# Kernel tuning notes

Hardware: AMD Instinct MI355X
Metric: run time of the kernel (lower is better)

## Reference

```python
import jax, jax.numpy as jnp
import numpy as np

B, T, A, G, E, H = 64, 128, 30, 3, 64, 256
FA, FE, NE = 32, 16, 30
LA = A * 36
SD = A * FA + NE * FE + LA  # 2520


def setup_inputs() -> dict:
    key = jax.random.key(0)
    ks = iter(jax.random.split(key, 64))
    p = lambda *s: jax.random.normal(next(ks), s, jnp.float32) * 0.02
    qvals = jax.random.normal(next(ks), (B, T, A), jnp.float32)
    # ally states with a valid one-hot group type in the last G slots (constant over t)
    ally = jax.random.normal(next(ks), (B, T, A, FA), jnp.float32)
    grp = jax.random.randint(next(ks), (B, A), 0, G)
    onehot = jax.nn.one_hot(grp, G, dtype=jnp.float32)  # (B,A,G)
    ally = ally.at[:, :, :, -G:].set(jnp.broadcast_to(onehot[:, None], (B, T, A, G)))
    rest = jax.random.normal(next(ks), (B, T, NE * FE + LA), jnp.float32)
    states = jnp.concatenate([ally.reshape(B, T, A * FA), rest], axis=2)
    d = {"qvals": qvals, "states": states}
    d["g_w1_W1"] = p(G, SD, H); d["g_w1_b1"] = p(G, H); d["g_w1_W2"] = p(G, H, A * E); d["g_w1_b2"] = p(G, A * E)
    d["g_b1_W1"] = p(G, SD, H); d["g_b1_b1"] = p(G, H); d["g_b1_W2"] = p(G, H, E); d["g_b1_b2"] = p(G, E)
    d["g_w2_W1"] = p(G, SD, H); d["g_w2_b1"] = p(G, H); d["g_w2_W2"] = p(G, H, E); d["g_w2_b2"] = p(G, E)
    d["g_b2_W1"] = p(G, SD, E); d["g_b2_b1"] = p(G, E); d["g_b2_W2"] = p(G, E, 1); d["g_b2_b2"] = p(G, 1)
    d["h_w1_W1"] = p(SD, H); d["h_w1_b1"] = p(H); d["h_w1_W2"] = p(H, G * E); d["h_w1_b2"] = p(G * E)
    d["h_b1_W1"] = p(SD, H); d["h_b1_b1"] = p(H); d["h_b1_W2"] = p(H, E); d["h_b1_b2"] = p(E)
    d["h_w2_W1"] = p(SD, H); d["h_w2_b1"] = p(H); d["h_w2_W2"] = p(H, E); d["h_w2_b2"] = p(E)
    d["h_b2_W1"] = p(SD, E); d["h_b2_b1"] = p(E); d["h_b2_W2"] = p(E, 1); d["h_b2_b2"] = p(1)
    return d


def reference(qvals, states,
              g_w1_W1, g_w1_b1, g_w1_W2, g_w1_b2,
              g_b1_W1, g_b1_b1, g_b1_W2, g_b1_b2,
              g_w2_W1, g_w2_b1, g_w2_W2, g_w2_b2,
              g_b2_W1, g_b2_b1, g_b2_W2, g_b2_b2,
              h_w1_W1, h_w1_b1, h_w1_W2, h_w1_b2,
              h_b1_W1, h_b1_b1, h_b1_W2, h_b1_b2,
              h_w2_W1, h_w2_b1, h_w2_W2, h_w2_b2,
              h_b2_W1, h_b2_b1, h_b2_W2, h_b2_b2):
    N = B * T
    s = states.reshape(N, SD)
    # group masks from the one-hot type slots at t=0 (constant across time)
    ally = states[..., : A * FA].reshape(B, T, A, FA)
    type0 = ally[:, 0, :, -G:]                                  # (B,A,G)
    masks = jnp.transpose(type0 == 1.0, (2, 0, 1)).astype(qvals.dtype)  # (G,B,A)
    mq = (qvals[None] * masks[:, :, None, :]).reshape(G, N, A)  # (G,N,A)

    def gmlp(W1, b1, W2, b2):  # stacked-over-groups 2-layer MLP
        h = jax.nn.relu(jnp.einsum('nd,gdh->gnh', s, W1) + b1[:, None])
        return jnp.einsum('gnh,gho->gno', h, W2) + b2[:, None]

    w1 = jnp.abs(gmlp(g_w1_W1, g_w1_b1, g_w1_W2, g_w1_b2)).reshape(G, N, A, E)
    b1 = gmlp(g_b1_W1, g_b1_b1, g_b1_W2, g_b1_b2)               # (G,N,E)
    w2 = jnp.abs(gmlp(g_w2_W1, g_w2_b1, g_w2_W2, g_w2_b2))      # (G,N,E)
    b2 = gmlp(g_b2_W1, g_b2_b1, g_b2_W2, g_b2_b2)[..., 0]       # (G,N)
    hidden = jax.nn.elu(jnp.einsum('gna,gnae->gne', mq, w1) + b1)
    group_qvals = (jnp.einsum('gne,gne->gn', hidden, w2) + b2).T  # (N,G)

    def hmlp(W1, b1_, W2, b2_):
        return jax.nn.relu(s @ W1 + b1_) @ W2 + b2_

    hw1 = jnp.abs(hmlp(h_w1_W1, h_w1_b1, h_w1_W2, h_w1_b2)).reshape(N, G, E)
    hb1 = hmlp(h_b1_W1, h_b1_b1, h_b1_W2, h_b1_b2)              # (N,E)
    hw2 = jnp.abs(hmlp(h_w2_W1, h_w2_b1, h_w2_W2, h_w2_b2))     # (N,E)
    hb2 = hmlp(h_b2_W1, h_b2_b1, h_b2_W2, h_b2_b2)[:, 0]        # (N,)
    hid = jax.nn.elu(jnp.einsum('ng,nge->ne', group_qvals, hw1) + hb1)
    qtot = jnp.einsum('ne,ne->n', hid, hw2) + hb2
    return qtot.reshape(B, T, 1)
```

## Files before the change

### kernel.cpp

```cpp
#include <hip/hip_runtime.h>

typedef unsigned short u16;
typedef __bf16 bf16x8 __attribute__((ext_vector_type(8)));
typedef float f32x4 __attribute__((ext_vector_type(4)));
typedef unsigned short u16x8 __attribute__((ext_vector_type(8)));

#define NB 64
#define NT 128
#define NA 30
#define NG 3
#define NE 64
#define NH 256
#define NN 8192
#define SD 2520
#define KP 2560
#define NC 3328
#define NKT 40
#define NITER 20

__device__ __forceinline__ u16 f2bf(float f) {
  union { float f; unsigned u; } c; c.f = f;
  unsigned u = c.u + 0x7FFFu + ((c.u >> 16) & 1u);
  return (u16)(u >> 16);
}
__device__ __forceinline__ float bf2f(u16 h) {
  union { unsigned u; float f; } c; c.u = ((unsigned)h) << 16;
  return c.f;
}
__device__ __forceinline__ float eluf(float x) { return x > 0.f ? x : expm1f(x); }

__device__ __forceinline__ void gload16(const u16* g, u16* l) {
  __builtin_amdgcn_global_load_lds((const __attribute__((address_space(1))) void*)g,
                                   (__attribute__((address_space(3))) void*)l, 16, 0, 0);
}

__device__ __forceinline__ float wredsum(float v) {
  #pragma unroll
  for (int d = 32; d > 0; d >>= 1) v += __shfl_xor(v, d, 64);
  return v;
}

__global__ __launch_bounds__(256) void pack_all_k(
    const float* __restrict__ states,
    const float* __restrict__ gw1W1, const float* __restrict__ gw1b1,
    const float* __restrict__ gb1W1, const float* __restrict__ gb1b1,
    const float* __restrict__ gw2W1, const float* __restrict__ gw2b1,
    const float* __restrict__ gb2W1, const float* __restrict__ gb2b1,
    const float* __restrict__ hw1W1, const float* __restrict__ hw1b1,
    const float* __restrict__ hb1W1, const float* __restrict__ hb1b1,
    const float* __restrict__ hw2W1, const float* __restrict__ hw2b1,
    const float* __restrict__ hb2W1, const float* __restrict__ hb2b1,
    const float* __restrict__ gw1W2, const float* __restrict__ gb1W2,
    const float* __restrict__ gw2W2, const float* __restrict__ hw1W2,
    const float* __restrict__ hb1W2, const float* __restrict__ hw2W2,
    u16* __restrict__ A, u16* __restrict__ BT, float* __restrict__ bias,
    u16* __restrict__ w2tw1, u16* __restrict__ w2ts,
    int* __restrict__ grps, int* __restrict__ gcnt) {
  int bid = blockIdx.x;
  if (bid < 10240) {
    int tid = bid * 256 + threadIdx.x;
    int n = tid / 320, kq = tid - n * 320;
    int k = kq * 8;
    u16x8 v;
    if (k < SD) {
      const float4* p = reinterpret_cast<const float4*>(states + (size_t)n * SD + k);
      float4 x0 = p[0], x1 = p[1];
      v[0]=f2bf(x0.x); v[1]=f2bf(x0.y); v[2]=f2bf(x0.z); v[3]=f2bf(x0.w);
      v[4]=f2bf(x1.x); v[5]=f2bf(x1.y); v[6]=f2bf(x1.z); v[7]=f2bf(x1.w);
    } else {
      v[0]=0;v[1]=0;v[2]=0;v[3]=0;v[4]=0;v[5]=0;v[6]=0;v[7]=0;
    }
    *reinterpret_cast<u16x8*>(A + (size_t)n * KP + k) = v;
  } else if (bid < 14400) {
    int tid = (bid - 10240) * 256 + threadIdx.x;
    int kq = tid / NC, j = tid - kq * NC;
    const float* W; const float* bsrc; size_t cbase; int stride; int q;
    if (j < 768)        { q=j;      int g=q>>8; W=gw1W1; cbase=(size_t)g*SD*NH + (q&255); stride=NH; bsrc=gw1b1; }
    else if (j < 1536)  { q=j-768;  int g=q>>8; W=gb1W1; cbase=(size_t)g*SD*NH + (q&255); stride=NH; bsrc=gb1b1; }
    else if (j < 2304)  { q=j-1536; int g=q>>8; W=gw2W1; cbase=(size_t)g*SD*NH + (q&255); stride=NH; bsrc=gw2b1; }
    else if (j < 2496)  { q=j-2304; int g=q>>6; W=gb2W1; cbase=(size_t)g*SD*NE + (q&63);  stride=NE; bsrc=gb2b1; }
    else if (j < 2752)  { q=j-2496; W=hw1W1; cbase=q; stride=NH; bsrc=hw1b1; }
    else if (j < 3008)  { q=j-2752; W=hb1W1; cbase=q; stride=NH; bsrc=hb1b1; }
    else if (j < 3264)  { q=j-3008; W=hw2W1; cbase=q; stride=NH; bsrc=hw2b1; }
    else                { q=j-3264; W=hb2W1; cbase=q; stride=NE; bsrc=hb2b1; }
    int k = kq * 8;
    u16x8 v;
    #pragma unroll
    for (int i = 0; i < 8; ++i) {
      int d = k + i;
      v[i] = (d < SD) ? f2bf(W[cbase + (size_t)d * stride]) : (u16)0;
    }
    *reinterpret_cast<u16x8*>(BT + (size_t)j * KP + k) = v;
    if (kq == 0) bias[j] = bsrc[q];
  } else if (bid < 15120) {
    int tid = (bid - 14400) * 256 + threadIdx.x;
    int lane = tid & 63, cf = (tid >> 6) & 3, ks = (tid >> 8) & 7, slab = tid >> 11;
    int g = slab / 30, a = slab - g * 30;
    int e = cf * 16 + (lane & 15);
    int h0 = ks * 32 + (lane >> 4) * 8;
    const float* src = gw1W2 + (size_t)g * (NH * 1920) + (size_t)h0 * 1920 + a * 64 + e;
    u16x8 v;
    #pragma unroll
    for (int i = 0; i < 8; ++i) v[i] = f2bf(src[(size_t)i * 1920]);
    *reinterpret_cast<u16x8*>(w2tw1 + (size_t)tid * 8) = v;
  } else if (bid < 15208) {
    int tid = (bid - 15120) * 256 + threadIdx.x;
    int lane = tid & 63, cf = (tid >> 6) & 3, ks = (tid >> 8) & 7, u = tid >> 11;
    int e = cf * 16 + (lane & 15);
    int h0 = ks * 32 + (lane >> 4) * 8;
    const float* src; int stride;
    if (u < 3)       { src = gb1W2 + (size_t)u * (NH*NE) + (size_t)h0 * NE + e;     stride = NE; }
    else if (u < 6)  { src = gw2W2 + (size_t)(u-3) * (NH*NE) + (size_t)h0 * NE + e; stride = NE; }
    else if (u < 9)  { src = hw1W2 + (size_t)h0 * (NG*NE) + (u-6)*64 + e;           stride = NG*NE; }
    else if (u == 9) { src = hb1W2 + (size_t)h0 * NE + e;                           stride = NE; }
    else             { src = hw2W2 + (size_t)h0 * NE + e;                           stride = NE; }
    u16x8 v;
    #pragma unroll
    for (int i = 0; i < 8; ++i) v[i] = f2bf(src[(size_t)i * stride]);
    *reinterpret_cast<u16x8*>(w2ts + (size_t)tid * 8) = v;
  } else {
    int b = threadIdx.x;
    if (b >= NB) return;
    int gv0 = 0, gv1 = 0;
    int cnt0 = 0, cnt1 = 0, cnt2 = 0;
    #pragma unroll
    for (int a = 0; a < NA; ++a) {
      int g = 0;
      #pragma unroll
      for (int gi = 0; gi < NG; ++gi)
        if (states[(size_t)b * NT * SD + a * 32 + 29 + gi] == 1.0f) g = gi;
      if (a < 15) gv0 |= g << (2 * a); else gv1 |= g << (2 * (a - 15));
      if (g == 0) ++cnt0; else if (g == 1) ++cnt1; else ++cnt2;
    }
    gcnt[b * 4 + 0] = cnt0; gcnt[b * 4 + 1] = cnt1; gcnt[b * 4 + 2] = cnt2;
    int off0 = 0, off1 = cnt0, off2 = cnt0 + cnt1;
    #pragma unroll
    for (int a = 0; a < NA; ++a) {
      int g = (a < 15) ? ((gv0 >> (2 * a)) & 3) : ((gv1 >> (2 * (a - 15))) & 3);
      int pos;
      if (g == 0) pos = off0++; else if (g == 1) pos = off1++; else pos = off2++;
      grps[b * NA + pos] = a;
    }
  }
}

__global__ __launch_bounds__(512, 2) void gemm1_k(const u16* __restrict__ A, const u16* __restrict__ BT,
    const float* __restrict__ bias, u16* __restrict__ act) {
  __shared__ u16 lds[65536];
  int t = threadIdx.x;
  int wg = blockIdx.x;
  int swz = (wg & 7) * 52 + (wg >> 3);
  int by = swz / 13, bx = swz - by * 13;
  size_t mb = (size_t)by * 256, nb = (size_t)bx * 256;
  int lane = t & 63, w = t >> 6;
  int wm = (w >> 2) * 128;
  int wn = (w & 3) * 64;
  int l15 = lane & 15, hi = lane >> 4;

  int srow = t >> 3;
  int scol = (((t & 7) ^ (srow & 7)) << 3);
  const u16* aS = A + (mb + srow) * KP + scol;
  const u16* bS = BT + (nb + srow) * KP + scol;

#define STGA(buf, h, kt) { \
    u16* d_ = lds + (buf) * 32768 + (h) * 8192; \
    const u16* s_ = aS + (size_t)((h) * 128) * KP + (size_t)(kt) * 64; \
    gload16(s_,                  d_ + t * 8); \
    gload16(s_ + (size_t)64 * KP, d_ + 4096 + t * 8); }
#define STGB(buf, h, kt) { \
    u16* d_ = lds + (buf) * 32768 + 16384 + (h) * 8192; \
    const u16* s_ = bS + (size_t)((h) * 128) * KP + (size_t)(kt) * 64; \
    gload16(s_,                  d_ + t * 8); \
    gload16(s_ + (size_t)64 * KP, d_ + 4096 + t * 8); }

  f32x4 acc[8][4];
  #pragma unroll
  for (int mi = 0; mi < 8; ++mi)
    #pragma unroll
    for (int ni = 0; ni < 4; ++ni) acc[mi][ni] = {0.f, 0.f, 0.f, 0.f};

  const char* A0 = (const char*)(lds) + (wm ? 16384 : 0);
  const char* B0 = (const char*)(lds) + 32768 + ((wn & 128) ? 16384 : 0);
  const char* A1 = A0 + 65536;
  const char* B1 = B0 + 65536;
  int rx = l15 & 7;
  int aBase = l15 * 128;
  int bBase = ((wn & 64) + l15) * 128;
  int slot0 = (hi ^ rx) << 4;
  int slot1 = ((4 + hi) ^ rx) << 4;

  bf16x8 afA[4][2], afB[4][2], bfA[2][2], bfB[2][2];

#define LD_AFA(Ab) { _Pragma("unroll") for (int m_ = 0; m_ < 4; ++m_) { \
    afA[m_][0] = *reinterpret_cast<const bf16x8*>((Ab) + aBase + m_ * 2048 + slot0); \
    afA[m_][1] = *reinterpret_cast<const bf16x8*>((Ab) + aBase + m_ * 2048 + slot1); } }
#define LD_AFB(Ab) { _Pragma("unroll") for (int m_ = 0; m_ < 4; ++m_) { \
    afB[m_][0] = *reinterpret_cast<const bf16x8*>((Ab) + aBase + (4 + m_) * 2048 + slot0); \
    afB[m_][1] = *reinterpret_cast<const bf16x8*>((Ab) + aBase + (4 + m_) * 2048 + slot1); } }
#define LD_BFA(Bb) { _Pragma("unroll") for (int n_ = 0; n_ < 2; ++n_) { \
    bfA[n_][0] = *reinterpret_cast<const bf16x8*>((Bb) + bBase + n_ * 2048 + slot0); \
    bfA[n_][1] = *reinterpret_cast<const bf16x8*>((Bb) + bBase + n_ * 2048 + slot1); } }
#define LD_BFB(Bb) { _Pragma("unroll") for (int n_ = 0; n_ < 2; ++n_) { \
    bfB[n_][0] = *reinterpret_cast<const bf16x8*>((Bb) + bBase + (2 + n_) * 2048 + slot0); \
    bfB[n_][1] = *reinterpret_cast<const bf16x8*>((Bb) + bBase + (2 + n_) * 2048 + slot1); } }
#define MM_Q(AF, BF, MO, NO) { _Pragma("unroll") for (int m_ = 0; m_ < 4; ++m_) \
    _Pragma("unroll") for (int n_ = 0; n_ < 2; ++n_) { \
      acc[(MO)+m_][(NO)+n_] = __builtin_amdgcn_mfma_f32_16x16x32_bf16(AF[m_][0], BF[n_][0], acc[(MO)+m_][(NO)+n_], 0, 0, 0); \
      acc[(MO)+m_][(NO)+n_] = __builtin_amdgcn_mfma_f32_16x16x32_bf16(AF[m_][1], BF[n_][1], acc[(MO)+m_][(NO)+n_], 0, 0, 0); } }
#define SYNC_IN  __builtin_amdgcn_s_barrier(); \
                 asm volatile("s_waitcnt lgkmcnt(0)" ::: "memory"); \
                 __builtin_amdgcn_sched_barrier(0); \
                 __builtin_amdgcn_s_setprio(1);
#define SYNC_OUT __builtin_amdgcn_s_setprio(0); \
                 __builtin_amdgcn_s_barrier(); \
                 asm volatile("" ::: "memory");

  STGA(0, 0, 0); STGA(0, 1, 0); STGB(0, 0, 0); STGB(0, 1, 0);
  STGB(1, 0, 1); STGB(1, 1, 1);
  asm volatile("s_waitcnt vmcnt(4)" ::: "memory");
  __builtin_amdgcn_s_barrier();
  asm volatile("" ::: "memory");

  for (int it = 0; it < NITER; ++it) {
    int k1 = 2 * it + 1;
    bool t2 = (2 * it + 2 < NKT), t3 = (2 * it + 3 < NKT);
    LD_AFA(A0); LD_BFA(B0);
    STGA(1, 0, k1);
    SYNC_IN; MM_Q(afA, bfA, 0, 0); SYNC_OUT;
    LD_BFB(B0);
    STGA(1, 1, k1);
    SYNC_IN; MM_Q(afA, bfB, 0, 2); SYNC_OUT;
    LD_AFB(A0);
    if (t2) STGB(0, 0, 2 * it + 2);
    SYNC_IN; MM_Q(afB, bfB, 4, 2); SYNC_OUT;
    if (t2) STGB(0, 1, 2 * it + 2);
    __builtin_amdgcn_s_barrier();
    __builtin_amdgcn_s_setprio(1); MM_Q(afB, bfA, 4, 0); __builtin_amdgcn_s_setprio(0);
    if (it == NITER - 1) { asm volatile("s_waitcnt vmcnt(0)" ::: "memory"); }
    else                 { asm volatile("s_waitcnt vmcnt(4)" ::: "memory"); }
    __builtin_amdgcn_s_barrier();
    asm volatile("" ::: "memory");
    LD_AFA(A1); LD_BFA(B1);
    if (t2) STGA(0, 0, 2 * it + 2);
    SYNC_IN; MM_Q(afA, bfA, 0, 0); SYNC_OUT;
    LD_BFB(B1);
    if (t2) STGA(0, 1, 2 * it + 2);
    SYNC_IN; MM_Q(afA, bfB, 0, 2); SYNC_OUT;
    LD_AFB(A1);
    if (t3) STGB(1, 0, 2 * it + 3);
    SYNC_IN; MM_Q(afB, bfB, 4, 2); SYNC_OUT;
    if (t3) STGB(1, 1, 2 * it + 3);
    __builtin_amdgcn_s_barrier();
    __builtin_amdgcn_s_setprio(1); MM_Q(afB, bfA, 4, 0); __builtin_amdgcn_s_setprio(0);
    if (t3) { asm volatile("s_waitcnt vmcnt(4)" ::: "memory"); }
    __builtin_amdgcn_s_barrier();
    asm volatile("" ::: "memory");
  }

  int r00 = (int)mb + wm + hi * 4;
  int cc0 = (int)nb + wn + l15;
  float bv0 = bias[cc0], bv1 = bias[cc0 + 16], bv2 = bias[cc0 + 32], bv3 = bias[cc0 + 48];
  #pragma unroll
  for (int mi = 0; mi < 8; ++mi) {
    #pragma unroll
    for (int i = 0; i < 4; ++i) {
      u16* dst = act + (size_t)(r00 + mi * 16 + i) * NC + cc0;
      float v0 = acc[mi][0][i] + bv0; v0 = v0 > 0.f ? v0 : 0.f;
      float v1 = acc[mi][1][i] + bv1; v1 = v1 > 0.f ? v1 : 0.f;
      float v2 = acc[mi][2][i] + bv2; v2 = v2 > 0.f ? v2 : 0.f;
      float v3 = acc[mi][3][i] + bv3; v3 = v3 > 0.f ? v3 : 0.f;
      dst[0] = f2bf(v0); dst[16] = f2bf(v1); dst[32] = f2bf(v2); dst[48] = f2bf(v3);
    }
  }
#undef STGA
#undef STGB
#undef LD_AFA
#undef LD_AFB
#undef LD_BFA
#undef LD_BFB
#undef MM_Q
#undef SYNC_IN
#undef SYNC_OUT
}

__global__ __launch_bounds__(128) void c1a_k(const u16* __restrict__ act, const float* __restrict__ qvals,
    const int* __restrict__ grps, const int* __restrict__ gcnt, const u16* __restrict__ w2tw1,
    const float* __restrict__ gw1b2, float* __restrict__ qw1acc) {
  int t = threadIdx.x, lane = t & 63, w = t >> 6;
  int rb = blockIdx.x;
  int g = blockIdx.y;
  int nb0 = rb * 32 + w * 16;
  int b = rb >> 2;
  int l16 = lane & 15, lk8 = (lane >> 4) * 8;
  int cnt0 = gcnt[b * 4], cnt1 = gcnt[b * 4 + 1], cnt2 = gcnt[b * 4 + 2];
  int start = (g >= 1 ? cnt0 : 0) + (g >= 2 ? cnt1 : 0);
  int cnt = (g == 0) ? cnt0 : (g == 1) ? cnt1 : cnt2;
  float gacc[4][4];
  #pragma unroll
  for (int cf = 0; cf < 4; ++cf)
    #pragma unroll
    for (int i = 0; i < 4; ++i) gacc[cf][i] = 0.f;
  const u16* arow = act + (size_t)(nb0 + l16) * NC;
  int r4 = nb0 + (lane >> 4) * 4;
  const u16* abase = arow + g * NH;
  bf16x8 af0[4], af1[4];
  #pragma unroll
  for (int ks = 0; ks < 4; ++ks) {
    af0[ks] = *reinterpret_cast<const bf16x8*>(abase + ks * 32 + lk8);
    af1[ks] = *reinterpret_cast<const bf16x8*>(abase + (4 + ks) * 32 + lk8);
  }
  const int* sl = grps + b * NA + start;
  for (int ai = 0; ai < cnt; ++ai) {
    int a = sl[ai];
    f32x4 t4[4], u4[4];
    #pragma unroll
    for (int cf = 0; cf < 4; ++cf) { t4[cf] = {0.f,0.f,0.f,0.f}; u4[cf] = {0.f,0.f,0.f,0.f}; }
    const u16* bbase = w2tw1 + (size_t)(g * NA + a) * 16384 + lane * 8;
    #pragma unroll
    for (int ks = 0; ks < 4; ++ks) {
      #pragma unroll
      for (int cf = 0; cf < 4; ++cf) {
        bf16x8 bf0 = *reinterpret_cast<const bf16x8*>(bbase + (ks * 4 + cf) * 512);
        bf16x8 bf1 = *reinterpret_cast<const bf16x8*>(bbase + ((4 + ks) * 4 + cf) * 512);
        t4[cf] = __builtin_amdgcn_mfma_f32_16x16x32_bf16(af0[ks], bf0, t4[cf], 0, 0, 0);
        u4[cf] = __builtin_amdgcn_mfma_f32_16x16x32_bf16(af1[ks], bf1, u4[cf], 0, 0, 0);
      }
    }
    float qv[4];
    #pragma unroll
    for (int i = 0; i < 4; ++i) qv[i] = qvals[(size_t)(r4 + i) * NA + a];
    const float* bias = gw1b2 + (size_t)g * (NA * NE) + a * NE;
    #pragma unroll
    for (int cf = 0; cf < 4; ++cf) {
      float bv = bias[cf*16 + l16];
      #pragma unroll
      for (int i = 0; i < 4; ++i) gacc[cf][i] += qv[i] * fabsf(t4[cf][i] + u4[cf][i] + bv);
    }
  }
  #pragma unroll
  for (int cf = 0; cf < 4; ++cf)
    #pragma unroll
    for (int i = 0; i < 4; ++i)
      qw1acc[(size_t)(r4 + i) * 192 + g * 64 + cf * 16 + l16] = gacc[cf][i];
}

__global__ __launch_bounds__(256) void c1b_k(const u16* __restrict__ act, const u16* __restrict__ w2ts,
    const float* __restrict__ gb1b2, const float* __restrict__ gw2b2, const float* __restrict__ hw1b2,
    const float* __restrict__ hb1b2, const float* __restrict__ hw2b2,
    float* __restrict__ b1s, float* __restrict__ w2s, float* __restrict__ hw1s,
    float* __restrict__ hb1s, float* __restrict__ hw2s) {
  int u = blockIdx.x, blk = blockIdx.y;
  int t = threadIdx.x, lane = t & 63, w = t >> 6;
  int nb0 = blk * 64 + w * 16;
  int l16 = lane & 15, lk8 = (lane >> 4) * 8;
  int aoff = (u < 3) ? 768 + u * 256 : (u < 6) ? 1536 + (u-3) * 256 : (u < 9) ? 2496 : (u == 9) ? 2752 : 3008;
  const float* bias; float* outp; int ostride; bool ab;
  if (u < 3)       { bias = gb1b2 + u * 64;       outp = b1s  + u * 64;     ostride = 192; ab = false; }
  else if (u < 6)  { bias = gw2b2 + (u-3) * 64;   outp = w2s  + (u-3) * 64; ostride = 192; ab = true; }
  else if (u < 9)  { bias = hw1b2 + (u-6) * 64;   outp = hw1s + (u-6) * 64; ostride = 192; ab = true; }
  else if (u == 9) { bias = hb1b2;                outp = hb1s;              ostride = 64;  ab = false; }
  else             { bias = hw2b2;                outp = hw2s;              ostride = 64;  ab = true; }
  f32x4 t4[4];
  #pragma unroll
  for (int cf = 0; cf < 4; ++cf) t4[cf] = {0.f, 0.f, 0.f, 0.f};
  const u16* arow = act + (size_t)(nb0 + l16) * NC + aoff;
  const u16* bbase = w2ts + (size_t)u * 16384 + lane * 8;
  #pragma unroll
  for (int ks = 0; ks < 8; ++ks) {
    bf16x8 af = *reinterpret_cast<const bf16x8*>(arow + ks * 32 + lk8);
    #pragma unroll
    for (int cf = 0; cf < 4; ++cf) {
      bf16x8 bf = *reinterpret_cast<const bf16x8*>(bbase + (ks * 4 + cf) * 512);
      t4[cf] = __builtin_amdgcn_mfma_f32_16x16x32_bf16(af, bf, t4[cf], 0, 0, 0);
    }
  }
  int r4 = nb0 + (lane >> 4) * 4;
  #pragma unroll
  for (int cf = 0; cf < 4; ++cf) {
    float bv = bias[cf*16 + l16];
    #pragma unroll
    for (int i = 0; i < 4; ++i) {
      float v = t4[cf][i] + bv;
      if (ab) v = fabsf(v);
      outp[(size_t)(r4 + i) * ostride + cf * 16 + l16] = v;
    }
  }
}

__global__ __launch_bounds__(256) void c2_k(const u16* __restrict__ act,
    const float* __restrict__ qw1acc, const float* __restrict__ b1s, const float* __restrict__ w2s,
    const float* __restrict__ hw1s, const float* __restrict__ hb1s, const float* __restrict__ hw2s,
    const float* __restrict__ gb2W2, const float* __restrict__ gb2b2,
    const float* __restrict__ hb2W2, const float* __restrict__ hb2b2,
    float* __restrict__ out) {
  int gtid = blockIdx.x * 256 + threadIdx.x;
  int n = gtid >> 6, e = gtid & 63;
  const u16* an = act + (size_t)n * NC;
  const float* qn = qw1acc + (size_t)n * 192;
  float q0 = qn[e], q1 = qn[64 + e], q2 = qn[128 + e];
  const float* b1n = b1s + (size_t)n * 192;
  const float* w2n = w2s + (size_t)n * 192;
  float s0 = bf2f(an[2304 + e]) * gb2W2[e]       + eluf(q0 + b1n[e])       * w2n[e];
  float s1 = bf2f(an[2368 + e]) * gb2W2[64 + e]  + eluf(q1 + b1n[64 + e])  * w2n[64 + e];
  float s2 = bf2f(an[2432 + e]) * gb2W2[128 + e] + eluf(q2 + b1n[128 + e]) * w2n[128 + e];
  float sh = bf2f(an[3264 + e]) * hb2W2[e];
  float gq0 = wredsum(s0) + gb2b2[0];
  float gq1 = wredsum(s1) + gb2b2[1];
  float gq2 = wredsum(s2) + gb2b2[2];
  float hb2v = wredsum(sh) + hb2b2[0];
  const float* hw1n = hw1s + (size_t)n * 192;
  float hv = gq0 * hw1n[e] + gq1 * hw1n[64 + e] + gq2 * hw1n[128 + e] + hb1s[(size_t)n * 64 + e];
  float c = eluf(hv) * hw2s[(size_t)n * 64 + e];
  float qt = wredsum(c) + hb2v;
  if (e == 0) out[n] = qt;
}

extern "C" void kernel_launch(void* const* d_in, const int* in_sizes, int n_in,
                              void* d_out, int out_size, void* d_ws, size_t ws_size,
                              hipStream_t stream) {
  const float* qvals  = (const float*)d_in[0];
  const float* states = (const float*)d_in[1];
  const float* gw1W1 = (const float*)d_in[2];
  const float* gw1b1 = (const float*)d_in[3];
  const float* gw1W2 = (const float*)d_in[4];
  const float* gw1b2 = (const float*)d_in[5];
  const float* gb1W1 = (const float*)d_in[6];
  const float* gb1b1 = (const float*)d_in[7];
  const float* gb1W2 = (const float*)d_in[8];
  const float* gb1b2 = (const float*)d_in[9];
  const float* gw2W1 = (const float*)d_in[10];
  const float* gw2b1 = (const float*)d_in[11];
  const float* gw2W2 = (const float*)d_in[12];
  const float* gw2b2 = (const float*)d_in[13];
  const float* gb2W1 = (const float*)d_in[14];
  const float* gb2b1 = (const float*)d_in[15];
  const float* gb2W2 = (const float*)d_in[16];
  const float* gb2b2 = (const float*)d_in[17];
  const float* hw1W1 = (const float*)d_in[18];
  const float* hw1b1 = (const float*)d_in[19];
  const float* hw1W2 = (const float*)d_in[20];
  const float* hw1b2 = (const float*)d_in[21];
  const float* hb1W1 = (const float*)d_in[22];
  const float* hb1b1 = (const float*)d_in[23];
  const float* hb1W2 = (const float*)d_in[24];
  const float* hb1b2 = (const float*)d_in[25];
  const float* hw2W1 = (const float*)d_in[26];
  const float* hw2b1 = (const float*)d_in[27];
  const float* hw2W2 = (const float*)d_in[28];
  const float* hw2b2 = (const float*)d_in[29];
  const float* hb2W1 = (const float*)d_in[30];
  const float* hb2b1 = (const float*)d_in[31];
  const float* hb2W2 = (const float*)d_in[32];
  const float* hb2b2 = (const float*)d_in[33];
  float* out = (float*)d_out;

  char* p = (char*)d_ws;
  u16* A       = (u16*)p;   p += (size_t)NN * KP * 2;
  u16* BT      = (u16*)p;   p += (size_t)NC * KP * 2;
  u16* act     = (u16*)p;   p += (size_t)NN * NC * 2;
  u16* w2tw1   = (u16*)p;   p += (size_t)5760 * NH * 2;
  u16* w2ts    = (u16*)p;   p += (size_t)704 * NH * 2;
  float* bias  = (float*)p; p += (size_t)NC * 4;
  int* grps    = (int*)p;   p += (size_t)NB * NA * 4;
  int* gcnt    = (int*)p;   p += (size_t)NB * 4 * 4;
  float* b1s   = (float*)p; p += (size_t)NN * 192 * 4;
  float* w2s   = (float*)p; p += (size_t)NN * 192 * 4;
  float* hw1s  = (float*)p; p += (size_t)NN * 192 * 4;
  float* hb1s  = (float*)p; p += (size_t)NN * 64 * 4;
  float* hw2s  = (float*)p; p += (size_t)NN * 64 * 4;
  float* qw1acc = (float*)A;

  pack_all_k<<<15209, 256, 0, stream>>>(states,
                                        gw1W1, gw1b1, gb1W1, gb1b1, gw2W1, gw2b1, gb2W1, gb2b1,
                                        hw1W1, hw1b1, hb1W1, hb1b1, hw2W1, hw2b1, hb2W1, hb2b1,
                                        gw1W2, gb1W2, gw2W2, hw1W2, hb1W2, hw2W2,
                                        A, BT, bias, w2tw1, w2ts, grps, gcnt);
  gemm1_k<<<416, 512, 0, stream>>>(A, BT, bias, act);
  c1a_k<<<dim3(256, 3), 128, 0, stream>>>(act, qvals, grps, gcnt, w2tw1, gw1b2, qw1acc);
  c1b_k<<<dim3(11, 128), 256, 0, stream>>>(act, w2ts, gb1b2, gw2b2, hw1b2, hb1b2, hw2b2,
                                           b1s, w2s, hw1s, hb1s, hw2s);
  c2_k<<<2048, 256, 0, stream>>>(act, qw1acc, b1s, w2s, hw1s, hb1s, hw2s,
                                 gb2W2, gb2b2, hb2W2, hb2b2, out);
}
```

Before: 237.2 us.

## Fuse second-layer hypernet GEMMs with final mixing into one kernel

Merges c1b_k and c2_k into a single kernel that computes the eleven small second-layer MFMA products per 16-row tile and consumes them directly in registers for the group and hyper mixing. The b2 dot products become an extra MFMA unit packed into w2ts, replacing the wave reductions. This removes the fp32 intermediate buffers (b1s, w2s, hw1s, hb1s, hw2s) and their global write and reread traffic, plus one launch. In exchange the fused kernel runs only 128 blocks with serial per-wave work, so parallelism and occupancy are much lower.

```diff
diff --git a/kernel.cpp b/kernel.cpp
--- a/kernel.cpp
+++ b/kernel.cpp
@@ -32,12 +32,6 @@
 __device__ __forceinline__ void gload16(const u16* g, u16* l) {
   __builtin_amdgcn_global_load_lds((const __attribute__((address_space(1))) void*)g,
                                    (__attribute__((address_space(3))) void*)l, 16, 0, 0);
-}
-
-__device__ __forceinline__ float wredsum(float v) {
-  #pragma unroll
-  for (int d = 32; d > 0; d >>= 1) v += __shfl_xor(v, d, 64);
-  return v;
 }
 
 __global__ __launch_bounds__(256) void pack_all_k(
@@ -53,6 +47,7 @@
     const float* __restrict__ gw1W2, const float* __restrict__ gb1W2,
     const float* __restrict__ gw2W2, const float* __restrict__ hw1W2,
     const float* __restrict__ hb1W2, const float* __restrict__ hw2W2,
+    const float* __restrict__ gb2W2, const float* __restrict__ hb2W2,
     u16* __restrict__ A, u16* __restrict__ BT, float* __restrict__ bias,
     u16* __restrict__ w2tw1, u16* __restrict__ w2ts,
     int* __restrict__ grps, int* __restrict__ gcnt) {
@@ -103,20 +98,31 @@
     #pragma unroll
     for (int i = 0; i < 8; ++i) v[i] = f2bf(src[(size_t)i * 1920]);
     *reinterpret_cast<u16x8*>(w2tw1 + (size_t)tid * 8) = v;
-  } else if (bid < 15208) {
+  } else if (bid < 15216) {
     int tid = (bid - 15120) * 256 + threadIdx.x;
     int lane = tid & 63, cf = (tid >> 6) & 3, ks = (tid >> 8) & 7, u = tid >> 11;
-    int e = cf * 16 + (lane & 15);
+    int c = cf * 16 + (lane & 15);
     int h0 = ks * 32 + (lane >> 4) * 8;
-    const float* src; int stride;
-    if (u < 3)       { src = gb1W2 + (size_t)u * (NH*NE) + (size_t)h0 * NE + e;     stride = NE; }
-    else if (u < 6)  { src = gw2W2 + (size_t)(u-3) * (NH*NE) + (size_t)h0 * NE + e; stride = NE; }
-    else if (u < 9)  { src = hw1W2 + (size_t)h0 * (NG*NE) + (u-6)*64 + e;           stride = NG*NE; }
-    else if (u == 9) { src = hb1W2 + (size_t)h0 * NE + e;                           stride = NE; }
-    else             { src = hw2W2 + (size_t)h0 * NE + e;                           stride = NE; }
     u16x8 v;
-    #pragma unroll
-    for (int i = 0; i < 8; ++i) v[i] = f2bf(src[(size_t)i * stride]);
+    if (u < 11) {
+      const float* src; int stride;
+      if (u < 3)       { src = gb1W2 + (size_t)u * (NH*NE) + (size_t)h0 * NE + c;     stride = NE; }
+      else if (u < 6)  { src = gw2W2 + (size_t)(u-3) * (NH*NE) + (size_t)h0 * NE + c; stride = NE; }
+      else if (u < 9)  { src = hw1W2 + (size_t)h0 * (NG*NE) + (u-6)*64 + c;           stride = NG*NE; }
+      else if (u == 9) { src = hb1W2 + (size_t)h0 * NE + c;                           stride = NE; }
+      else             { src = hw2W2 + (size_t)h0 * NE + c;                           stride = NE; }
+      #pragma unroll
+      for (int i = 0; i < 8; ++i) v[i] = f2bf(src[(size_t)i * stride]);
+    } else {
+      #pragma unroll
+      for (int i = 0; i < 8; ++i) {
+        int k = h0 + i;
+        float val = 0.f;
+        if (ks < 6) { if (c == k / 64) val = gb2W2[k]; }
+        else        { int kk = k - 192; if (c == 3) val = hb2W2[kk]; }
+        v[i] = f2bf(val);
+      }
+    }
     *reinterpret_cast<u16x8*>(w2ts + (size_t)tid * 8) = v;
   } else {
     int b = threadIdx.x;
@@ -344,75 +350,121 @@
       qw1acc[(size_t)(r4 + i) * 192 + g * 64 + cf * 16 + l16] = gacc[cf][i];
 }
 
-__global__ __launch_bounds__(256) void c1b_k(const u16* __restrict__ act, const u16* __restrict__ w2ts,
+__global__ __launch_bounds__(256) void c1bc2_k(const u16* __restrict__ act,
+    const float* __restrict__ qw1acc, const u16* __restrict__ w2ts,
     const float* __restrict__ gb1b2, const float* __restrict__ gw2b2, const float* __restrict__ hw1b2,
     const float* __restrict__ hb1b2, const float* __restrict__ hw2b2,
-    float* __restrict__ b1s, float* __restrict__ w2s, float* __restrict__ hw1s,
-    float* __restrict__ hb1s, float* __restrict__ hw2s) {
-  int u = blockIdx.x, blk = blockIdx.y;
+    const float* __restrict__ gb2b2, const float* __restrict__ hb2b2,
+    float* __restrict__ out) {
   int t = threadIdx.x, lane = t & 63, w = t >> 6;
-  int nb0 = blk * 64 + w * 16;
-  int l16 = lane & 15, lk8 = (lane >> 4) * 8;
-  int aoff = (u < 3) ? 768 + u * 256 : (u < 6) ? 1536 + (u-3) * 256 : (u < 9) ? 2496 : (u == 9) ? 2752 : 3008;
-  const float* bias; float* outp; int ostride; bool ab;
-  if (u < 3)       { bias = gb1b2 + u * 64;       outp = b1s  + u * 64;     ostride = 192; ab = false; }
-  else if (u < 6)  { bias = gw2b2 + (u-3) * 64;   outp = w2s  + (u-3) * 64; ostride = 192; ab = true; }
-  else if (u < 9)  { bias = hw1b2 + (u-6) * 64;   outp = hw1s + (u-6) * 64; ostride = 192; ab = true; }
-  else if (u == 9) { bias = hb1b2;                outp = hb1s;              ostride = 64;  ab = false; }
-  else             { bias = hw2b2;                outp = hw2s;              ostride = 64;  ab = true; }
-  f32x4 t4[4];
-  #pragma unroll
-  for (int cf = 0; cf < 4; ++cf) t4[cf] = {0.f, 0.f, 0.f, 0.f};
-  const u16* arow = act + (size_t)(nb0 + l16) * NC + aoff;
-  const u16* bbase = w2ts + (size_t)u * 16384 + lane * 8;
-  #pragma unroll
-  for (int ks = 0; ks < 8; ++ks) {
-    bf16x8 af = *reinterpret_cast<const bf16x8*>(arow + ks * 32 + lk8);
+  int nb0 = blockIdx.x * 64 + w * 16;
+  int l16 = lane & 15, hi = lane >> 4, lk8 = hi * 8;
+  const u16* arow = act + (size_t)(nb0 + l16) * NC;
+  int r4 = nb0 + hi * 4;
+
+#define UNIT(u_, aoff_, res_) { \
+    f32x4 t4_[4]; \
+    _Pragma("unroll") for (int cf = 0; cf < 4; ++cf) t4_[cf] = {0.f,0.f,0.f,0.f}; \
+    const u16* bb_ = w2ts + (size_t)(u_) * 16384 + lane * 8; \
+    _Pragma("unroll") for (int ks = 0; ks < 8; ++ks) { \
+      bf16x8 af_ = *reinterpret_cast<const bf16x8*>(arow + (aoff_) + ks * 32 + lk8); \
+      _Pragma("unroll") for (int cf = 0; cf < 4; ++cf) { \
+        bf16x8 bf_ = *reinterpret_cast<const bf16x8*>(bb_ + (ks * 4 + cf) * 512); \
+        t4_[cf] = __builtin_amdgcn_mfma_f32_16x16x32_bf16(af_, bf_, t4_[cf], 0, 0, 0); \
+      } } \
+    _Pragma("unroll") for (int cf = 0; cf < 4; ++cf) res_[cf] = t4_[cf]; }
+
+#define GRED(x) { x += __shfl_xor(x, 1, 64); x += __shfl_xor(x, 2, 64); \
+                  x += __shfl_xor(x, 4, 64); x += __shfl_xor(x, 8, 64); }
+
+  f32x4 d4 = {0.f, 0.f, 0.f, 0.f};
+  {
+    const u16* bb = w2ts + (size_t)11 * 16384 + lane * 8;
+    #pragma unroll
+    for (int ks = 0; ks < 8; ++ks) {
+      int aoff = (ks < 6) ? (2304 + ks * 32) : (3264 + (ks - 6) * 32);
+      bf16x8 af = *reinterpret_cast<const bf16x8*>(arow + aoff + lk8);
+      bf16x8 bf = *reinterpret_cast<const bf16x8*>(bb + (ks * 4) * 512);
+      d4 = __builtin_amdgcn_mfma_f32_16x16x32_bf16(af, bf, d4, 0, 0, 0);
+    }
+  }
+  float dotn[4][4];
+  #pragma unroll
+  for (int n = 0; n < 4; ++n)
+    #pragma unroll
+    for (int i = 0; i < 4; ++i)
+      dotn[n][i] = __shfl(d4[i], (lane & 48) + n, 64);
+
+  float gq[3][4];
+  #pragma unroll
+  for (int g = 0; g < 3; ++g) {
+    f32x4 b1r[4], w2r[4];
+    UNIT(g, 768 + g * 256, b1r);
+    UNIT(3 + g, 1536 + g * 256, w2r);
+    float part[4] = {0.f, 0.f, 0.f, 0.f};
     #pragma unroll
     for (int cf = 0; cf < 4; ++cf) {
-      bf16x8 bf = *reinterpret_cast<const bf16x8*>(bbase + (ks * 4 + cf) * 512);
-      t4[cf] = __builtin_amdgcn_mfma_f32_16x16x32_bf16(af, bf, t4[cf], 0, 0, 0);
-    }
-  }
-  int r4 = nb0 + (lane >> 4) * 4;
+      float b1b = gb1b2[g * 64 + cf * 16 + l16];
+      float w2b = gw2b2[g * 64 + cf * 16 + l16];
+      #pragma unroll
+      for (int i = 0; i < 4; ++i) {
+        float q = qw1acc[(size_t)(r4 + i) * 192 + g * 64 + cf * 16 + l16];
+        part[i] += eluf(q + b1r[cf][i] + b1b) * fabsf(w2r[cf][i] + w2b);
+      }
+    }
+    #pragma unroll
+    for (int i = 0; i < 4; ++i) {
+      GRED(part[i]);
+      gq[g][i] = part[i] + dotn[g][i] + gb2b2[g];
+    }
+  }
+
+  f32x4 h6[4], h7[4], h8[4], h9[4], h10[4];
+  {
+    f32x4 t6[4], t7[4], t8[4];
+    #pragma unroll
+    for (int cf = 0; cf < 4; ++cf) { t6[cf] = {0.f,0.f,0.f,0.f}; t7[cf] = {0.f,0.f,0.f,0.f}; t8[cf] = {0.f,0.f,0.f,0.f}; }
+    const u16* bb6 = w2ts + (size_t)6 * 16384 + lane * 8;
+    const u16* bb7 = w2ts + (size_t)7 * 16384 + lane * 8;
+    const u16* bb8 = w2ts + (size_t)8 * 16384 + lane * 8;
+    #pragma unroll
+    for (int ks = 0; ks < 8; ++ks) {
+      bf16x8 af = *reinterpret_cast<const bf16x8*>(arow + 2496 + ks * 32 + lk8);
+      #pragma unroll
+      for (int cf = 0; cf < 4; ++cf) {
+        t6[cf] = __builtin_amdgcn_mfma_f32_16x16x32_bf16(af, *reinterpret_cast<const bf16x8*>(bb6 + (ks*4+cf)*512), t6[cf], 0, 0, 0);
+        t7[cf] = __builtin_amdgcn_mfma_f32_16x16x32_bf16(af, *reinterpret_cast<const bf16x8*>(bb7 + (ks*4+cf)*512), t7[cf], 0, 0, 0);
+        t8[cf] = __builtin_amdgcn_mfma_f32_16x16x32_bf16(af, *reinterpret_cast<const bf16x8*>(bb8 + (ks*4+cf)*512), t8[cf], 0, 0, 0);
+      }
+    }
+    #pragma unroll
+    for (int cf = 0; cf < 4; ++cf) { h6[cf] = t6[cf]; h7[cf] = t7[cf]; h8[cf] = t8[cf]; }
+  }
+  UNIT(9, 2752, h9);
+  UNIT(10, 3008, h10);
+
+  float qtp[4] = {0.f, 0.f, 0.f, 0.f};
   #pragma unroll
   for (int cf = 0; cf < 4; ++cf) {
-    float bv = bias[cf*16 + l16];
+    int e = cf * 16 + l16;
+    float b6 = hw1b2[e], b7 = hw1b2[64 + e], b8 = hw1b2[128 + e];
+    float b9 = hb1b2[e], b10 = hw2b2[e];
     #pragma unroll
     for (int i = 0; i < 4; ++i) {
-      float v = t4[cf][i] + bv;
-      if (ab) v = fabsf(v);
-      outp[(size_t)(r4 + i) * ostride + cf * 16 + l16] = v;
-    }
-  }
-}
-
-__global__ __launch_bounds__(256) void c2_k(const u16* __restrict__ act,
-    const float* __restrict__ qw1acc, const float* __restrict__ b1s, const float* __restrict__ w2s,
-    const float* __restrict__ hw1s, const float* __restrict__ hb1s, const float* __restrict__ hw2s,
-    const float* __restrict__ gb2W2, const float* __restrict__ gb2b2,
-    const float* __restrict__ hb2W2, const float* __restrict__ hb2b2,
-    float* __restrict__ out) {
-  int gtid = blockIdx.x * 256 + threadIdx.x;
-  int n = gtid >> 6, e = gtid & 63;
-  const u16* an = act + (size_t)n * NC;
-  const float* qn = qw1acc + (size_t)n * 192;
-  float q0 = qn[e], q1 = qn[64 + e], q2 = qn[128 + e];
-  const float* b1n = b1s + (size_t)n * 192;
-  const float* w2n = w2s + (size_t)n * 192;
-  float s0 = bf2f(an[2304 + e]) * gb2W2[e]       + eluf(q0 + b1n[e])       * w2n[e];
-  float s1 = bf2f(an[2368 + e]) * gb2W2[64 + e]  + eluf(q1 + b1n[64 + e])  * w2n[64 + e];
-  float s2 = bf2f(an[2432 + e]) * gb2W2[128 + e] + eluf(q2 + b1n[128 + e]) * w2n[128 + e];
-  float sh = bf2f(an[3264 + e]) * hb2W2[e];
-  float gq0 = wredsum(s0) + gb2b2[0];
-  float gq1 = wredsum(s1) + gb2b2[1];
-  float gq2 = wredsum(s2) + gb2b2[2];
-  float hb2v = wredsum(sh) + hb2b2[0];
-  const float* hw1n = hw1s + (size_t)n * 192;
-  float hv = gq0 * hw1n[e] + gq1 * hw1n[64 + e] + gq2 * hw1n[128 + e] + hb1s[(size_t)n * 64 + e];
-  float c = eluf(hv) * hw2s[(size_t)n * 64 + e];
-  float qt = wredsum(c) + hb2v;
-  if (e == 0) out[n] = qt;
+      float hv = gq[0][i] * fabsf(h6[cf][i] + b6)
+               + gq[1][i] * fabsf(h7[cf][i] + b7)
+               + gq[2][i] * fabsf(h8[cf][i] + b8)
+               + h9[cf][i] + b9;
+      qtp[i] += eluf(hv) * fabsf(h10[cf][i] + b10);
+    }
+  }
+  #pragma unroll
+  for (int i = 0; i < 4; ++i) {
+    GRED(qtp[i]);
+    if (l16 == 0) out[r4 + i] = qtp[i] + dotn[3][i] + hb2b2[0];
+  }
+#undef UNIT
+#undef GRED
 }
 
 extern "C" void kernel_launch(void* const* d_in, const int* in_sizes, int n_in,
@@ -459,26 +511,19 @@
   u16* BT      = (u16*)p;   p += (size_t)NC * KP * 2;
   u16* act     = (u16*)p;   p += (size_t)NN * NC * 2;
   u16* w2tw1   = (u16*)p;   p += (size_t)5760 * NH * 2;
-  u16* w2ts    = (u16*)p;   p += (size_t)704 * NH * 2;
+  u16* w2ts    = (u16*)p;   p += (size_t)12 * 16384 * 2;
   float* bias  = (float*)p; p += (size_t)NC * 4;
   int* grps    = (int*)p;   p += (size_t)NB * NA * 4;
   int* gcnt    = (int*)p;   p += (size_t)NB * 4 * 4;
-  float* b1s   = (float*)p; p += (size_t)NN * 192 * 4;
-  float* w2s   = (float*)p; p += (size_t)NN * 192 * 4;
-  float* hw1s  = (float*)p; p += (size_t)NN * 192 * 4;
-  float* hb1s  = (float*)p; p += (size_t)NN * 64 * 4;
-  float* hw2s  = (float*)p; p += (size_t)NN * 64 * 4;
   float* qw1acc = (float*)A;
 
-  pack_all_k<<<15209, 256, 0, stream>>>(states,
+  pack_all_k<<<15217, 256, 0, stream>>>(states,
                                         gw1W1, gw1b1, gb1W1, gb1b1, gw2W1, gw2b1, gb2W1, gb2b1,
                                         hw1W1, hw1b1, hb1W1, hb1b1, hw2W1, hw2b1, hb2W1, hb2b1,
-                                        gw1W2, gb1W2, gw2W2, hw1W2, hb1W2, hw2W2,
+                                        gw1W2, gb1W2, gw2W2, hw1W2, hb1W2, hw2W2, gb2W2, hb2W2,
                                         A, BT, bias, w2tw1, w2ts, grps, gcnt);
   gemm1_k<<<416, 512, 0, stream>>>(A, BT, bias, act);
   c1a_k<<<dim3(256, 3), 128, 0, stream>>>(act, qvals, grps, gcnt, w2tw1, gw1b2, qw1acc);
-  c1b_k<<<dim3(11, 128), 256, 0, stream>>>(act, w2ts, gb1b2, gw2b2, hw1b2, hb1b2, hw2b2,
-                                           b1s, w2s, hw1s, hb1s, hw2s);
-  c2_k<<<2048, 256, 0, stream>>>(act, qw1acc, b1s, w2s, hw1s, hb1s, hw2s,
-                                 gb2W2, gb2b2, hb2W2, hb2b2, out);
-}
+  c1bc2_k<<<128, 256, 0, stream>>>(act, qw1acc, w2ts, gb1b2, gw2b2, hw1b2, hb1b2, hw2b2,
+                                   gb2b2, hb2b2, out);
+}
```

New measurement: 294.6 us. 24.2% more time.
